# Kernel optimization log

Measured on AMD Instinct MI355X. Metric: run time of the kernel, lower is better.

Reference implementation:

```python
import jax, jax.numpy as jnp
import numpy as np

EPS = 1e-5

def _bn_eval(x, gamma, beta, mean, var):
    return (x - mean) * (gamma / jnp.sqrt(var + EPS)) + beta

def setup_inputs() -> dict:
    key = jax.random.key(0)
    ks = jax.random.split(key, 12)
    N, E, D, C, H = 100000, 1000000, 64, 32, 128
    fused = 4 * D + C  # 288
    z = jax.random.normal(ks[0], (N, D), dtype=jnp.float32)
    edge_index = jax.random.randint(ks[1], (2, E), 0, N, dtype=jnp.int64)
    edge_context = jax.random.normal(ks[2], (E, C), dtype=jnp.float32)
    W1 = jax.random.normal(ks[3], (fused, H), dtype=jnp.float32) / np.sqrt(fused)
    b1 = jnp.zeros((H,), jnp.float32)
    g1 = jnp.ones((H,), jnp.float32); be1 = jnp.zeros((H,), jnp.float32)
    m1 = jnp.zeros((H,), jnp.float32); v1 = jnp.ones((H,), jnp.float32)
    W2 = jax.random.normal(ks[4], (H, H // 2), dtype=jnp.float32) / np.sqrt(H)
    b2 = jnp.zeros((H // 2,), jnp.float32)
    g2 = jnp.ones((H // 2,), jnp.float32); be2 = jnp.zeros((H // 2,), jnp.float32)
    m2 = jnp.zeros((H // 2,), jnp.float32); v2 = jnp.ones((H // 2,), jnp.float32)
    W3 = jax.random.normal(ks[5], (H // 2, 1), dtype=jnp.float32) / np.sqrt(H // 2)
    b3 = jnp.zeros((1,), jnp.float32)
    return {"z": z, "edge_index": edge_index, "edge_context": edge_context,
            "W1": W1, "b1": b1, "g1": g1, "be1": be1, "m1": m1, "v1": v1,
            "W2": W2, "b2": b2, "g2": g2, "be2": be2, "m2": m2, "v2": v2,
            "W3": W3, "b3": b3}

def reference(z, edge_index, edge_context,
              W1, b1, g1, be1, m1, v1,
              W2, b2, g2, be2, m2, v2,
              W3, b3):
    # gather endpoint embeddings: [E, D]
    src = z[edge_index[0]]
    dst = z[edge_index[1]]
    # fused features: [E, 4*D + C]
    fused = jnp.concatenate([src, dst, src * dst, jnp.abs(src - dst), edge_context], axis=1)
    x = jax.nn.relu(_bn_eval(fused @ W1 + b1, g1, be1, m1, v1))
    x = jax.nn.relu(_bn_eval(x @ W2 + b2, g2, be2, m2, v2))
    return (x @ W3 + b3).reshape(-1)
```

## Files before the change

kernel.cpp:

```cpp
#include <hip/hip_runtime.h>
#include <hip/hip_bf16.h>

typedef __attribute__((ext_vector_type(8))) short bf16x8;
typedef __attribute__((ext_vector_type(4))) float f32x4;
typedef __attribute__((ext_vector_type(4))) unsigned int u32x4;
typedef __attribute__((ext_vector_type(2))) unsigned int u32x2;
typedef __attribute__((ext_vector_type(2))) __bf16 bf16x2v;

#define EPS 1e-5f

__device__ inline unsigned short f2bf(float x) {
  unsigned int u = __builtin_bit_cast(unsigned int, x);
  unsigned int r = (u + 0x7FFFu + ((u >> 16) & 1u)) >> 16;
  return (unsigned short)r;
}

__device__ inline unsigned int cvtpk(float a, float b) {
  bf16x2v v = {(__bf16)a, (__bf16)b};
  return __builtin_bit_cast(unsigned int, v);
}

__global__ void prep_kernel(const float* __restrict__ W1, const float* __restrict__ W2,
                            const float* __restrict__ b1, const float* __restrict__ g1,
                            const float* __restrict__ be1, const float* __restrict__ m1,
                            const float* __restrict__ v1,
                            const float* __restrict__ b2, const float* __restrict__ g2,
                            const float* __restrict__ be2, const float* __restrict__ m2,
                            const float* __restrict__ v2,
                            unsigned short* __restrict__ w1f, unsigned short* __restrict__ w2f,
                            float* __restrict__ sc) {
  int t = blockIdx.x * 256 + threadIdx.x;
  if (t < 36864) {
    int j = t & 7, l = (t >> 3) & 63, f = t >> 9;
    int kb = f >> 3, nb = f & 7;
    int rk = kb * 32 + ((l >> 4) << 3) + j;
    int cn = (nb << 4) + (l & 15);
    w1f[t] = f2bf(W1[rk * 128 + cn]);
  } else if (t < 45056) {
    int o = t - 36864;
    int j = o & 7, l = (o >> 3) & 63, f = o >> 9;
    int kb = f >> 2, nb = f & 3;
    int s = kb * 32 + ((l >> 4) << 3) + j;
    int rk = (s & 96) | ((s & 1) << 4) | ((s >> 1) & 15);
    int cn = (nb << 4) + (l & 15);
    w2f[o] = f2bf(W2[rk * 64 + cn]);
  } else if (t < 45184) {
    int j = t - 45056;
    float s = g1[j] * rsqrtf(v1[j] + EPS);
    sc[j] = s;
    sc[128 + j] = (b1[j] - m1[j]) * s + be1[j];
  } else if (t < 45248) {
    int j = t - 45184;
    float s = g2[j] * rsqrtf(v2[j] + EPS);
    sc[256 + j] = s;
    sc[320 + j] = (b2[j] - m2[j]) * s + be2[j];
  }
}

#define LDS_SC_OFF 73728
#define LDS_A_OFF 75776
#define LDS_L3_OFF 157696
#define LDS_TOTAL 158720

#define WRITE_A()                                                                                \
  do {                                                                                           \
    const int rswz_ = (sr & 7) << 4;                                                             \
    char* rowp_ = AR + sr * 640;                                                                 \
    u32x4 ps_ = {cvtpk(sv0[0], sv0[1]), cvtpk(sv0[2], sv0[3]), cvtpk(sv1[0], sv1[1]),            \
                 cvtpk(sv1[2], sv1[3])};                                                         \
    u32x4 pd_ = {cvtpk(dv0[0], dv0[1]), cvtpk(dv0[2], dv0[3]), cvtpk(dv1[0], dv1[1]),            \
                 cvtpk(dv1[2], dv1[3])};                                                         \
    u32x4 pp_ = {cvtpk(sv0[0] * dv0[0], sv0[1] * dv0[1]), cvtpk(sv0[2] * dv0[2], sv0[3] * dv0[3]),\
                 cvtpk(sv1[0] * dv1[0], sv1[1] * dv1[1]), cvtpk(sv1[2] * dv1[2], sv1[3] * dv1[3])};\
    u32x4 pa_ = {cvtpk(fabsf(sv0[0] - dv0[0]), fabsf(sv0[1] - dv0[1])),                          \
                 cvtpk(fabsf(sv0[2] - dv0[2]), fabsf(sv0[3] - dv0[3])),                          \
                 cvtpk(fabsf(sv1[0] - dv1[0]), fabsf(sv1[1] - dv1[1])),                          \
                 cvtpk(fabsf(sv1[2] - dv1[2]), fabsf(sv1[3] - dv1[3]))};                         \
    u32x2 pc_ = {cvtpk(cv[0], cv[1]), cvtpk(cv[2], cv[3])};                                      \
    *(u32x4*)(rowp_ + ((sh * 16) ^ rswz_)) = ps_;                                                \
    *(u32x4*)(rowp_ + ((128 + sh * 16) ^ rswz_)) = pd_;                                          \
    *(u32x4*)(rowp_ + ((256 + sh * 16) ^ rswz_)) = pp_;                                          \
    *(u32x4*)(rowp_ + ((384 + sh * 16) ^ rswz_)) = pa_;                                          \
    *(u32x2*)(rowp_ + 512 + ((sh * 8) ^ rswz_)) = pc_;                                           \
  } while (0)

#define GATHER_NEXT(tg)                                                                          \
  do {                                                                                           \
    const f32x4* zs_ = (const f32x4*)(z + ((size_t)i0n * 64 + sh * 8));                          \
    sv0 = zs_[0];                                                                                \
    sv1 = zs_[1];                                                                                \
    const f32x4* zd_ = (const f32x4*)(z + ((size_t)i1n * 64 + sh * 8));                          \
    dv0 = zd_[0];                                                                                \
    dv1 = zd_[1];                                                                                \
    int eg_ = ((tg) << 7) + sr;                                                                  \
    int esg_ = eg_ < E ? eg_ : E - 1;                                                            \
    cv = *(const f32x4*)(ctx + (size_t)esg_ * 32 + sh * 4);                                      \
    int tn_ = (tg) + grid;                                                                       \
    if (tn_ >= nblk) tn_ = (tg);                                                                 \
    int en_ = (tn_ << 7) + sr;                                                                   \
    int esn_ = en_ < E ? en_ : E - 1;                                                            \
    i0n = ei[esn_];                                                                              \
    i1n = ei[E + esn_];                                                                          \
  } while (0)

__global__ __launch_bounds__(1024, 4) void fused_kernel(
    const float* __restrict__ z, const int* __restrict__ ei, const float* __restrict__ ctx,
    const unsigned short* __restrict__ w1f, const unsigned short* __restrict__ w2f,
    const float* __restrict__ sc, const float* __restrict__ w3, const float* __restrict__ b3,
    float* __restrict__ out, int E, int nblk) {
  extern __shared__ char lds[];
  char* W1L = lds;
  float* SC = (float*)(lds + LDS_SC_OFF);
  char* AR = lds + LDS_A_OFF;
  char* X1 = lds + LDS_A_OFF;
  float* l3 = (float*)(lds + LDS_L3_OFF);

  const int tid = threadIdx.x;
  const int lane = tid & 63, wave = tid >> 6;
  const int g = lane >> 4, lq = lane & 15;
  const int wr = wave >> 2, wc = wave & 3;
  const int w2r = wave >> 1, w2c = wave & 1;
  const int sr = tid >> 3, sh = tid & 7;
  const int grid = gridDim.x;

  {
    const f32x4* s = (const f32x4*)w1f;
    f32x4* d = (f32x4*)W1L;
#pragma unroll
    for (int i = 0; i < 4; i++) d[i * 1024 + tid] = s[i * 1024 + tid];
    if (tid < 512) d[4096 + tid] = s[4096 + tid];
    if (tid < 128) {
      SC[tid] = sc[tid];
      SC[128 + tid] = sc[128 + tid];
    } else if (tid < 192) {
      int j = tid - 128;
      SC[256 + j] = sc[256 + j];
      SC[320 + j] = sc[320 + j];
      SC[384 + j] = w3[j];
    } else if (tid == 192) {
      SC[448] = b3[0];
    }
  }

  bf16x8 w2g0, w2g1, w2g2, w2g3, w2h0, w2h1, w2h2, w2h3;
  {
    const bf16x8* W2G = (const bf16x8*)w2f;
    w2g0 = W2G[(0 * 4 + w2c * 2 + 0) * 64 + lane];
    w2h0 = W2G[(0 * 4 + w2c * 2 + 1) * 64 + lane];
    w2g1 = W2G[(1 * 4 + w2c * 2 + 0) * 64 + lane];
    w2h1 = W2G[(1 * 4 + w2c * 2 + 1) * 64 + lane];
    w2g2 = W2G[(2 * 4 + w2c * 2 + 0) * 64 + lane];
    w2h2 = W2G[(2 * 4 + w2c * 2 + 1) * 64 + lane];
    w2g3 = W2G[(3 * 4 + w2c * 2 + 0) * 64 + lane];
    w2h3 = W2G[(3 * 4 + w2c * 2 + 1) * 64 + lane];
  }

  f32x4 sv0, sv1, dv0, dv1, cv;
  int i0n, i1n;
  int t = blockIdx.x;

  {
    int e = (t << 7) + sr;
    int es = e < E ? e : E - 1;
    int a0 = ei[es], a1 = ei[E + es];
    cv = *(const f32x4*)(ctx + (size_t)es * 32 + sh * 4);
    const f32x4* zs = (const f32x4*)(z + ((size_t)a0 * 64 + sh * 8));
    sv0 = zs[0];
    sv1 = zs[1];
    const f32x4* zd = (const f32x4*)(z + ((size_t)a1 * 64 + sh * 8));
    dv0 = zd[0];
    dv1 = zd[1];
    int tn = t + grid;
    if (tn >= nblk) tn = t;
    int en = (tn << 7) + sr;
    int esn = en < E ? en : E - 1;
    i0n = ei[esn];
    i1n = ei[E + esn];
  }
  WRITE_A();
  {
    int tn = t + grid;
    if (tn >= nblk) tn = t;
    GATHER_NEXT(tn);
  }
  __syncthreads();

  for (; t < nblk; t += grid) {
    f32x4 acc00 = {0.f, 0.f, 0.f, 0.f}, acc01 = acc00, acc10 = acc00, acc11 = acc00;
    const bf16x8* W1F = (const bf16x8*)W1L;
    const int row0 = wr * 32 + lq, row1 = row0 + 16;
    const int swz0 = (row0 & 7) << 4, swz1 = (row1 & 7) << 4;
    const char* ap0 = AR + row0 * 640;
    const char* ap1 = AR + row1 * 640;
#pragma unroll
    for (int kb = 0; kb < 9; kb++) {
      bf16x8 a0 = *(const bf16x8*)(ap0 + ((kb * 64 + g * 16) ^ swz0));
      bf16x8 a1 = *(const bf16x8*)(ap1 + ((kb * 64 + g * 16) ^ swz1));
      bf16x8 b0 = W1F[(kb * 8 + wc * 2 + 0) * 64 + lane];
      bf16x8 b1 = W1F[(kb * 8 + wc * 2 + 1) * 64 + lane];
      acc00 = __builtin_amdgcn_mfma_f32_16x16x32_bf16(a0, b0, acc00, 0, 0, 0);
      acc01 = __builtin_amdgcn_mfma_f32_16x16x32_bf16(a0, b1, acc01, 0, 0, 0);
      acc10 = __builtin_amdgcn_mfma_f32_16x16x32_bf16(a1, b0, acc10, 0, 0, 0);
      acc11 = __builtin_amdgcn_mfma_f32_16x16x32_bf16(a1, b1, acc11, 0, 0, 0);
    }
    __syncthreads();

    {
      const int col0 = wc * 32 + lq, col1 = col0 + 16;
      const float s1v0 = SC[col0], c1v0 = SC[128 + col0];
      const float s1v1 = SC[col1], c1v1 = SC[128 + col1];
      const int xoff = wc * 64 + lq * 4;
#pragma unroll
      for (int j = 0; j < 4; j++) {
        int rowa = wr * 32 + 4 * g + j;
        unsigned int pA = cvtpk(fmaxf(acc00[j] * s1v0 + c1v0, 0.f),
                                fmaxf(acc01[j] * s1v1 + c1v1, 0.f));
        *(unsigned int*)(X1 + rowa * 256 + (xoff ^ ((rowa & 7) << 4))) = pA;
        int rowb = rowa + 16;
        unsigned int pB = cvtpk(fmaxf(acc10[j] * s1v0 + c1v0, 0.f),
                                fmaxf(acc11[j] * s1v1 + c1v1, 0.f));
        *(unsigned int*)(X1 + rowb * 256 + (xoff ^ ((rowb & 7) << 4))) = pB;
      }
    }
    __syncthreads();

    f32x4 acc2A = {0.f, 0.f, 0.f, 0.f}, acc2B = acc2A;
    {
      const int row = w2r * 16 + lq;
      const int swz = (row & 7) << 4;
      const char* xp = X1 + row * 256;
      bf16x8 a0 = *(const bf16x8*)(xp + ((0 * 64 + g * 16) ^ swz));
      acc2A = __builtin_amdgcn_mfma_f32_16x16x32_bf16(a0, w2g0, acc2A, 0, 0, 0);
      acc2B = __builtin_amdgcn_mfma_f32_16x16x32_bf16(a0, w2h0, acc2B, 0, 0, 0);
      bf16x8 a1 = *(const bf16x8*)(xp + ((1 * 64 + g * 16) ^ swz));
      acc2A = __builtin_amdgcn_mfma_f32_16x16x32_bf16(a1, w2g1, acc2A, 0, 0, 0);
      acc2B = __builtin_amdgcn_mfma_f32_16x16x32_bf16(a1, w2h1, acc2B, 0, 0, 0);
      bf16x8 a2 = *(const bf16x8*)(xp + ((2 * 64 + g * 16) ^ swz));
      acc2A = __builtin_amdgcn_mfma_f32_16x16x32_bf16(a2, w2g2, acc2A, 0, 0, 0);
      acc2B = __builtin_amdgcn_mfma_f32_16x16x32_bf16(a2, w2h2, acc2B, 0, 0, 0);
      bf16x8 a3 = *(const bf16x8*)(xp + ((3 * 64 + g * 16) ^ swz));
      acc2A = __builtin_amdgcn_mfma_f32_16x16x32_bf16(a3, w2g3, acc2A, 0, 0, 0);
      acc2B = __builtin_amdgcn_mfma_f32_16x16x32_bf16(a3, w2h3, acc2B, 0, 0, 0);
    }

    const int colA = w2c * 32 + lq, colB = colA + 16;
    const float s2A = SC[256 + colA], c2A = SC[320 + colA];
    const float s2B = SC[256 + colB], c2B = SC[320 + colB];
    const float w3A = SC[384 + colA], w3B = SC[384 + colB];
#pragma unroll
    for (int j = 0; j < 4; j++) {
      float vA = fmaxf(acc2A[j] * s2A + c2A, 0.f);
      float vB = fmaxf(acc2B[j] * s2B + c2B, 0.f);
      float p = vA * w3A + vB * w3B;
      p += __shfl_xor(p, 1);
      p += __shfl_xor(p, 2);
      p += __shfl_xor(p, 4);
      p += __shfl_xor(p, 8);
      if (lq == 0) l3[(w2r * 16 + 4 * g + j) * 2 + w2c] = p;
    }
    __syncthreads();

    WRITE_A();
    {
      int tn2 = t + 2 * grid;
      if (tn2 >= nblk) tn2 = t + grid < nblk ? t + grid : t;
      GATHER_NEXT(tn2);
    }
    if (tid < 128) {
      int e = (t << 7) + tid;
      if (e < E) out[e] = l3[tid * 2] + l3[tid * 2 + 1] + SC[448];
    }
    __syncthreads();
  }
}

extern "C" void kernel_launch(void* const* d_in, const int* in_sizes, int n_in,
                              void* d_out, int out_size, void* d_ws, size_t ws_size,
                              hipStream_t stream) {
  const float* z = (const float*)d_in[0];
  const int* ei = (const int*)d_in[1];
  const float* ctx = (const float*)d_in[2];
  const float* W1 = (const float*)d_in[3];
  const float* b1 = (const float*)d_in[4];
  const float* g1 = (const float*)d_in[5];
  const float* be1 = (const float*)d_in[6];
  const float* m1 = (const float*)d_in[7];
  const float* v1 = (const float*)d_in[8];
  const float* W2 = (const float*)d_in[9];
  const float* b2 = (const float*)d_in[10];
  const float* g2 = (const float*)d_in[11];
  const float* be2 = (const float*)d_in[12];
  const float* m2 = (const float*)d_in[13];
  const float* v2 = (const float*)d_in[14];
  const float* W3 = (const float*)d_in[15];
  const float* b3 = (const float*)d_in[16];
  float* out = (float*)d_out;
  const int E = out_size;

  unsigned short* w1f = (unsigned short*)d_ws;
  unsigned short* w2f = (unsigned short*)((char*)d_ws + 73728);
  float* sc = (float*)((char*)d_ws + 90112);

  prep_kernel<<<177, 256, 0, stream>>>(W1, W2, b1, g1, be1, m1, v1,
                                       b2, g2, be2, m2, v2, w1f, w2f, sc);

  const int nblk = (E + 127) >> 7;
  (void)hipFuncSetAttribute((const void*)fused_kernel,
                            hipFuncAttributeMaxDynamicSharedMemorySize, LDS_TOTAL);
  fused_kernel<<<256, 1024, LDS_TOTAL, stream>>>(z, ei, ctx, w1f, w2f, sc, W3, b3,
                                                 out, E, nblk);
}
```

Baseline: 137.7 us.

## Hold W1 in registers and halve block size with larger per-wave tiles

The W1 fragments move from shared memory into per-wave registers, so the weight matrix is no longer staged in LDS. Blocks shrink from 1024 to 512 threads, and each wave now computes 64 rows by 32 columns for layer 1 and 32 rows for layer 2. Each thread gathers twice as many embedding elements. Layer-1 activation writes are moved after the next-tile gather issue, and one barrier is dropped, so gather latency overlaps with compute. The cost is much higher register pressure (18 W1 plus 8 W2 fragments and 8 accumulators), which could cause spills or lower occupancy.

```diff
diff --git a/kernel.cpp b/kernel.cpp
--- a/kernel.cpp
+++ b/kernel.cpp
@@ -57,44 +57,58 @@
   }
 }
 
-#define LDS_SC_OFF 73728
-#define LDS_A_OFF 75776
-#define LDS_L3_OFF 157696
-#define LDS_TOTAL 158720
+#define LDS_X1_OFF 81920
+#define LDS_SC_OFF 114688
+#define LDS_L3_OFF 116736
+#define LDS_TOTAL 117760
 
 #define WRITE_A()                                                                                \
   do {                                                                                           \
     const int rswz_ = (sr & 7) << 4;                                                             \
     char* rowp_ = AR + sr * 640;                                                                 \
-    u32x4 ps_ = {cvtpk(sv0[0], sv0[1]), cvtpk(sv0[2], sv0[3]), cvtpk(sv1[0], sv1[1]),            \
+    u32x4 s0_ = {cvtpk(sv0[0], sv0[1]), cvtpk(sv0[2], sv0[3]), cvtpk(sv1[0], sv1[1]),            \
                  cvtpk(sv1[2], sv1[3])};                                                         \
-    u32x4 pd_ = {cvtpk(dv0[0], dv0[1]), cvtpk(dv0[2], dv0[3]), cvtpk(dv1[0], dv1[1]),            \
+    u32x4 s1_ = {cvtpk(sv2[0], sv2[1]), cvtpk(sv2[2], sv2[3]), cvtpk(sv3[0], sv3[1]),            \
+                 cvtpk(sv3[2], sv3[3])};                                                         \
+    u32x4 d0_ = {cvtpk(dv0[0], dv0[1]), cvtpk(dv0[2], dv0[3]), cvtpk(dv1[0], dv1[1]),            \
                  cvtpk(dv1[2], dv1[3])};                                                         \
-    u32x4 pp_ = {cvtpk(sv0[0] * dv0[0], sv0[1] * dv0[1]), cvtpk(sv0[2] * dv0[2], sv0[3] * dv0[3]),\
+    u32x4 d1_ = {cvtpk(dv2[0], dv2[1]), cvtpk(dv2[2], dv2[3]), cvtpk(dv3[0], dv3[1]),            \
+                 cvtpk(dv3[2], dv3[3])};                                                         \
+    u32x4 p0_ = {cvtpk(sv0[0] * dv0[0], sv0[1] * dv0[1]), cvtpk(sv0[2] * dv0[2], sv0[3] * dv0[3]),\
                  cvtpk(sv1[0] * dv1[0], sv1[1] * dv1[1]), cvtpk(sv1[2] * dv1[2], sv1[3] * dv1[3])};\
-    u32x4 pa_ = {cvtpk(fabsf(sv0[0] - dv0[0]), fabsf(sv0[1] - dv0[1])),                          \
+    u32x4 p1_ = {cvtpk(sv2[0] * dv2[0], sv2[1] * dv2[1]), cvtpk(sv2[2] * dv2[2], sv2[3] * dv2[3]),\
+                 cvtpk(sv3[0] * dv3[0], sv3[1] * dv3[1]), cvtpk(sv3[2] * dv3[2], sv3[3] * dv3[3])};\
+    u32x4 a0_ = {cvtpk(fabsf(sv0[0] - dv0[0]), fabsf(sv0[1] - dv0[1])),                          \
                  cvtpk(fabsf(sv0[2] - dv0[2]), fabsf(sv0[3] - dv0[3])),                          \
                  cvtpk(fabsf(sv1[0] - dv1[0]), fabsf(sv1[1] - dv1[1])),                          \
                  cvtpk(fabsf(sv1[2] - dv1[2]), fabsf(sv1[3] - dv1[3]))};                         \
-    u32x2 pc_ = {cvtpk(cv[0], cv[1]), cvtpk(cv[2], cv[3])};                                      \
-    *(u32x4*)(rowp_ + ((sh * 16) ^ rswz_)) = ps_;                                                \
-    *(u32x4*)(rowp_ + ((128 + sh * 16) ^ rswz_)) = pd_;                                          \
-    *(u32x4*)(rowp_ + ((256 + sh * 16) ^ rswz_)) = pp_;                                          \
-    *(u32x4*)(rowp_ + ((384 + sh * 16) ^ rswz_)) = pa_;                                          \
-    *(u32x2*)(rowp_ + 512 + ((sh * 8) ^ rswz_)) = pc_;                                           \
+    u32x4 a1_ = {cvtpk(fabsf(sv2[0] - dv2[0]), fabsf(sv2[1] - dv2[1])),                          \
+                 cvtpk(fabsf(sv2[2] - dv2[2]), fabsf(sv2[3] - dv2[3])),                          \
+                 cvtpk(fabsf(sv3[0] - dv3[0]), fabsf(sv3[1] - dv3[1])),                          \
+                 cvtpk(fabsf(sv3[2] - dv3[2]), fabsf(sv3[3] - dv3[3]))};                         \
+    u32x4 c0_ = {cvtpk(cv0[0], cv0[1]), cvtpk(cv0[2], cv0[3]), cvtpk(cv1[0], cv1[1]),            \
+                 cvtpk(cv1[2], cv1[3])};                                                         \
+    *(u32x4*)(rowp_ + ((sh * 32) ^ rswz_)) = s0_;                                                \
+    *(u32x4*)(rowp_ + ((sh * 32 + 16) ^ rswz_)) = s1_;                                           \
+    *(u32x4*)(rowp_ + ((128 + sh * 32) ^ rswz_)) = d0_;                                          \
+    *(u32x4*)(rowp_ + ((128 + sh * 32 + 16) ^ rswz_)) = d1_;                                     \
+    *(u32x4*)(rowp_ + ((256 + sh * 32) ^ rswz_)) = p0_;                                          \
+    *(u32x4*)(rowp_ + ((256 + sh * 32 + 16) ^ rswz_)) = p1_;                                     \
+    *(u32x4*)(rowp_ + ((384 + sh * 32) ^ rswz_)) = a0_;                                          \
+    *(u32x4*)(rowp_ + ((384 + sh * 32 + 16) ^ rswz_)) = a1_;                                     \
+    *(u32x4*)(rowp_ + ((512 + sh * 16) ^ rswz_)) = c0_;                                          \
   } while (0)
 
 #define GATHER_NEXT(tg)                                                                          \
   do {                                                                                           \
-    const f32x4* zs_ = (const f32x4*)(z + ((size_t)i0n * 64 + sh * 8));                          \
-    sv0 = zs_[0];                                                                                \
-    sv1 = zs_[1];                                                                                \
-    const f32x4* zd_ = (const f32x4*)(z + ((size_t)i1n * 64 + sh * 8));                          \
-    dv0 = zd_[0];                                                                                \
-    dv1 = zd_[1];                                                                                \
+    const f32x4* zs_ = (const f32x4*)(z + ((size_t)i0n * 64 + sh * 16));                         \
+    sv0 = zs_[0]; sv1 = zs_[1]; sv2 = zs_[2]; sv3 = zs_[3];                                      \
+    const f32x4* zd_ = (const f32x4*)(z + ((size_t)i1n * 64 + sh * 16));                         \
+    dv0 = zd_[0]; dv1 = zd_[1]; dv2 = zd_[2]; dv3 = zd_[3];                                      \
     int eg_ = ((tg) << 7) + sr;                                                                  \
     int esg_ = eg_ < E ? eg_ : E - 1;                                                            \
-    cv = *(const f32x4*)(ctx + (size_t)esg_ * 32 + sh * 4);                                      \
+    const f32x4* cx_ = (const f32x4*)(ctx + (size_t)esg_ * 32 + sh * 8);                         \
+    cv0 = cx_[0]; cv1 = cx_[1];                                                                  \
     int tn_ = (tg) + grid;                                                                       \
     if (tn_ >= nblk) tn_ = (tg);                                                                 \
     int en_ = (tn_ << 7) + sr;                                                                   \
@@ -103,16 +117,48 @@
     i1n = ei[E + esn_];                                                                          \
   } while (0)
 
-__global__ __launch_bounds__(1024, 4) void fused_kernel(
+#define MFMA16(A, B, C) __builtin_amdgcn_mfma_f32_16x16x32_bf16((A), (B), (C), 0, 0, 0)
+
+#define L1STEP(KB, BB0, BB1)                                                                     \
+  do {                                                                                           \
+    bf16x8 a0_ = *(const bf16x8*)(ap0 + (((KB) * 64 + g * 16) ^ aswz));                          \
+    bf16x8 a1_ = *(const bf16x8*)(ap1 + (((KB) * 64 + g * 16) ^ aswz));                          \
+    bf16x8 a2_ = *(const bf16x8*)(ap2 + (((KB) * 64 + g * 16) ^ aswz));                          \
+    bf16x8 a3_ = *(const bf16x8*)(ap3 + (((KB) * 64 + g * 16) ^ aswz));                          \
+    acc00 = MFMA16(a0_, BB0, acc00); acc01 = MFMA16(a0_, BB1, acc01);                            \
+    acc10 = MFMA16(a1_, BB0, acc10); acc11 = MFMA16(a1_, BB1, acc11);                            \
+    acc20 = MFMA16(a2_, BB0, acc20); acc21 = MFMA16(a2_, BB1, acc21);                            \
+    acc30 = MFMA16(a3_, BB0, acc30); acc31 = MFMA16(a3_, BB1, acc31);                            \
+  } while (0)
+
+#define X1W(MF, ACA, ACB)                                                                        \
+  do {                                                                                           \
+    _Pragma("unroll")                                                                            \
+    for (int j = 0; j < 4; j++) {                                                                \
+      int row_ = wr * 64 + (MF) * 16 + 4 * g + j;                                                \
+      unsigned int p_ = cvtpk(fmaxf(ACA[j] * s1v0 + c1v0, 0.f),                                  \
+                              fmaxf(ACB[j] * s1v1 + c1v1, 0.f));                                 \
+      *(unsigned int*)(X1 + row_ * 256 + (xoff ^ ((row_ & 7) << 4))) = p_;                       \
+    }                                                                                            \
+  } while (0)
+
+#define L2STEP(KB, WG, WH)                                                                       \
+  do {                                                                                           \
+    bf16x8 xa_ = *(const bf16x8*)(xp0 + (((KB) * 64 + g * 16) ^ aswz));                          \
+    bf16x8 xb_ = *(const bf16x8*)(xp1 + (((KB) * 64 + g * 16) ^ aswz));                          \
+    acc2A0 = MFMA16(xa_, WG, acc2A0); acc2A1 = MFMA16(xa_, WH, acc2A1);                          \
+    acc2B0 = MFMA16(xb_, WG, acc2B0); acc2B1 = MFMA16(xb_, WH, acc2B1);                          \
+  } while (0)
+
+__global__ __launch_bounds__(512, 2) void fused_kernel(
     const float* __restrict__ z, const int* __restrict__ ei, const float* __restrict__ ctx,
     const unsigned short* __restrict__ w1f, const unsigned short* __restrict__ w2f,
     const float* __restrict__ sc, const float* __restrict__ w3, const float* __restrict__ b3,
     float* __restrict__ out, int E, int nblk) {
   extern __shared__ char lds[];
-  char* W1L = lds;
+  char* AR = lds;
+  char* X1 = lds + LDS_X1_OFF;
   float* SC = (float*)(lds + LDS_SC_OFF);
-  char* AR = lds + LDS_A_OFF;
-  char* X1 = lds + LDS_A_OFF;
   float* l3 = (float*)(lds + LDS_L3_OFF);
 
   const int tid = threadIdx.x;
@@ -120,42 +166,40 @@
   const int g = lane >> 4, lq = lane & 15;
   const int wr = wave >> 2, wc = wave & 3;
   const int w2r = wave >> 1, w2c = wave & 1;
-  const int sr = tid >> 3, sh = tid & 7;
+  const int sr = tid >> 2, sh = tid & 3;
   const int grid = gridDim.x;
-
-  {
-    const f32x4* s = (const f32x4*)w1f;
-    f32x4* d = (f32x4*)W1L;
-#pragma unroll
-    for (int i = 0; i < 4; i++) d[i * 1024 + tid] = s[i * 1024 + tid];
-    if (tid < 512) d[4096 + tid] = s[4096 + tid];
-    if (tid < 128) {
-      SC[tid] = sc[tid];
-      SC[128 + tid] = sc[128 + tid];
-    } else if (tid < 192) {
-      int j = tid - 128;
-      SC[256 + j] = sc[256 + j];
-      SC[320 + j] = sc[320 + j];
-      SC[384 + j] = w3[j];
-    } else if (tid == 192) {
-      SC[448] = b3[0];
-    }
-  }
-
-  bf16x8 w2g0, w2g1, w2g2, w2g3, w2h0, w2h1, w2h2, w2h3;
-  {
-    const bf16x8* W2G = (const bf16x8*)w2f;
-    w2g0 = W2G[(0 * 4 + w2c * 2 + 0) * 64 + lane];
-    w2h0 = W2G[(0 * 4 + w2c * 2 + 1) * 64 + lane];
-    w2g1 = W2G[(1 * 4 + w2c * 2 + 0) * 64 + lane];
-    w2h1 = W2G[(1 * 4 + w2c * 2 + 1) * 64 + lane];
-    w2g2 = W2G[(2 * 4 + w2c * 2 + 0) * 64 + lane];
-    w2h2 = W2G[(2 * 4 + w2c * 2 + 1) * 64 + lane];
-    w2g3 = W2G[(3 * 4 + w2c * 2 + 0) * 64 + lane];
-    w2h3 = W2G[(3 * 4 + w2c * 2 + 1) * 64 + lane];
-  }
-
-  f32x4 sv0, sv1, dv0, dv1, cv;
+  const int aswz = (lq & 7) << 4;
+
+  if (tid < 128) {
+    SC[tid] = sc[tid];
+    SC[128 + tid] = sc[128 + tid];
+  } else if (tid < 192) {
+    int j = tid - 128;
+    SC[256 + j] = sc[256 + j];
+    SC[320 + j] = sc[320 + j];
+    SC[384 + j] = w3[j];
+  } else if (tid == 192) {
+    SC[448] = b3[0];
+  }
+
+  const bf16x8* W1G = (const bf16x8*)w1f;
+  bf16x8 w1r0 = W1G[(0 * 8 + wc * 2 + 0) * 64 + lane], w1s0 = W1G[(0 * 8 + wc * 2 + 1) * 64 + lane];
+  bf16x8 w1r1 = W1G[(1 * 8 + wc * 2 + 0) * 64 + lane], w1s1 = W1G[(1 * 8 + wc * 2 + 1) * 64 + lane];
+  bf16x8 w1r2 = W1G[(2 * 8 + wc * 2 + 0) * 64 + lane], w1s2 = W1G[(2 * 8 + wc * 2 + 1) * 64 + lane];
+  bf16x8 w1r3 = W1G[(3 * 8 + wc * 2 + 0) * 64 + lane], w1s3 = W1G[(3 * 8 + wc * 2 + 1) * 64 + lane];
+  bf16x8 w1r4 = W1G[(4 * 8 + wc * 2 + 0) * 64 + lane], w1s4 = W1G[(4 * 8 + wc * 2 + 1) * 64 + lane];
+  bf16x8 w1r5 = W1G[(5 * 8 + wc * 2 + 0) * 64 + lane], w1s5 = W1G[(5 * 8 + wc * 2 + 1) * 64 + lane];
+  bf16x8 w1r6 = W1G[(6 * 8 + wc * 2 + 0) * 64 + lane], w1s6 = W1G[(6 * 8 + wc * 2 + 1) * 64 + lane];
+  bf16x8 w1r7 = W1G[(7 * 8 + wc * 2 + 0) * 64 + lane], w1s7 = W1G[(7 * 8 + wc * 2 + 1) * 64 + lane];
+  bf16x8 w1r8 = W1G[(8 * 8 + wc * 2 + 0) * 64 + lane], w1s8 = W1G[(8 * 8 + wc * 2 + 1) * 64 + lane];
+
+  const bf16x8* W2G = (const bf16x8*)w2f;
+  bf16x8 w2g0 = W2G[(0 * 4 + w2c * 2 + 0) * 64 + lane], w2h0 = W2G[(0 * 4 + w2c * 2 + 1) * 64 + lane];
+  bf16x8 w2g1 = W2G[(1 * 4 + w2c * 2 + 0) * 64 + lane], w2h1 = W2G[(1 * 4 + w2c * 2 + 1) * 64 + lane];
+  bf16x8 w2g2 = W2G[(2 * 4 + w2c * 2 + 0) * 64 + lane], w2h2 = W2G[(2 * 4 + w2c * 2 + 1) * 64 + lane];
+  bf16x8 w2g3 = W2G[(3 * 4 + w2c * 2 + 0) * 64 + lane], w2h3 = W2G[(3 * 4 + w2c * 2 + 1) * 64 + lane];
+
+  f32x4 sv0, sv1, sv2, sv3, dv0, dv1, dv2, dv3, cv0, cv1;
   int i0n, i1n;
   int t = blockIdx.x;
 
@@ -163,13 +207,12 @@
     int e = (t << 7) + sr;
     int es = e < E ? e : E - 1;
     int a0 = ei[es], a1 = ei[E + es];
-    cv = *(const f32x4*)(ctx + (size_t)es * 32 + sh * 4);
-    const f32x4* zs = (const f32x4*)(z + ((size_t)a0 * 64 + sh * 8));
-    sv0 = zs[0];
-    sv1 = zs[1];
-    const f32x4* zd = (const f32x4*)(z + ((size_t)a1 * 64 + sh * 8));
-    dv0 = zd[0];
-    dv1 = zd[1];
+    const f32x4* cx = (const f32x4*)(ctx + (size_t)es * 32 + sh * 8);
+    cv0 = cx[0]; cv1 = cx[1];
+    const f32x4* zs = (const f32x4*)(z + ((size_t)a0 * 64 + sh * 16));
+    sv0 = zs[0]; sv1 = zs[1]; sv2 = zs[2]; sv3 = zs[3];
+    const f32x4* zd = (const f32x4*)(z + ((size_t)a1 * 64 + sh * 16));
+    dv0 = zd[0]; dv1 = zd[1]; dv2 = zd[2]; dv3 = zd[3];
     int tn = t + grid;
     if (tn >= nblk) tn = t;
     int en = (tn << 7) + sr;
@@ -187,77 +230,20 @@
 
   for (; t < nblk; t += grid) {
     f32x4 acc00 = {0.f, 0.f, 0.f, 0.f}, acc01 = acc00, acc10 = acc00, acc11 = acc00;
-    const bf16x8* W1F = (const bf16x8*)W1L;
-    const int row0 = wr * 32 + lq, row1 = row0 + 16;
-    const int swz0 = (row0 & 7) << 4, swz1 = (row1 & 7) << 4;
-    const char* ap0 = AR + row0 * 640;
-    const char* ap1 = AR + row1 * 640;
-#pragma unroll
-    for (int kb = 0; kb < 9; kb++) {
-      bf16x8 a0 = *(const bf16x8*)(ap0 + ((kb * 64 + g * 16) ^ swz0));
-      bf16x8 a1 = *(const bf16x8*)(ap1 + ((kb * 64 + g * 16) ^ swz1));
-      bf16x8 b0 = W1F[(kb * 8 + wc * 2 + 0) * 64 + lane];
-      bf16x8 b1 = W1F[(kb * 8 + wc * 2 + 1) * 64 + lane];
-      acc00 = __builtin_amdgcn_mfma_f32_16x16x32_bf16(a0, b0, acc00, 0, 0, 0);
-      acc01 = __builtin_amdgcn_mfma_f32_16x16x32_bf16(a0, b1, acc01, 0, 0, 0);
-      acc10 = __builtin_amdgcn_mfma_f32_16x16x32_bf16(a1, b0, acc10, 0, 0, 0);
-      acc11 = __builtin_amdgcn_mfma_f32_16x16x32_bf16(a1, b1, acc11, 0, 0, 0);
-    }
-    __syncthreads();
-
-    {
-      const int col0 = wc * 32 + lq, col1 = col0 + 16;
-      const float s1v0 = SC[col0], c1v0 = SC[128 + col0];
-      const float s1v1 = SC[col1], c1v1 = SC[128 + col1];
-      const int xoff = wc * 64 + lq * 4;
-#pragma unroll
-      for (int j = 0; j < 4; j++) {
-        int rowa = wr * 32 + 4 * g + j;
-        unsigned int pA = cvtpk(fmaxf(acc00[j] * s1v0 + c1v0, 0.f),
-                                fmaxf(acc01[j] * s1v1 + c1v1, 0.f));
-        *(unsigned int*)(X1 + rowa * 256 + (xoff ^ ((rowa & 7) << 4))) = pA;
-        int rowb = rowa + 16;
-        unsigned int pB = cvtpk(fmaxf(acc10[j] * s1v0 + c1v0, 0.f),
-                                fmaxf(acc11[j] * s1v1 + c1v1, 0.f));
-        *(unsigned int*)(X1 + rowb * 256 + (xoff ^ ((rowb & 7) << 4))) = pB;
-      }
-    }
-    __syncthreads();
-
-    f32x4 acc2A = {0.f, 0.f, 0.f, 0.f}, acc2B = acc2A;
-    {
-      const int row = w2r * 16 + lq;
-      const int swz = (row & 7) << 4;
-      const char* xp = X1 + row * 256;
-      bf16x8 a0 = *(const bf16x8*)(xp + ((0 * 64 + g * 16) ^ swz));
-      acc2A = __builtin_amdgcn_mfma_f32_16x16x32_bf16(a0, w2g0, acc2A, 0, 0, 0);
-      acc2B = __builtin_amdgcn_mfma_f32_16x16x32_bf16(a0, w2h0, acc2B, 0, 0, 0);
-      bf16x8 a1 = *(const bf16x8*)(xp + ((1 * 64 + g * 16) ^ swz));
-      acc2A = __builtin_amdgcn_mfma_f32_16x16x32_bf16(a1, w2g1, acc2A, 0, 0, 0);
-      acc2B = __builtin_amdgcn_mfma_f32_16x16x32_bf16(a1, w2h1, acc2B, 0, 0, 0);
-      bf16x8 a2 = *(const bf16x8*)(xp + ((2 * 64 + g * 16) ^ swz));
-      acc2A = __builtin_amdgcn_mfma_f32_16x16x32_bf16(a2, w2g2, acc2A, 0, 0, 0);
-      acc2B = __builtin_amdgcn_mfma_f32_16x16x32_bf16(a2, w2h2, acc2B, 0, 0, 0);
-      bf16x8 a3 = *(const bf16x8*)(xp + ((3 * 64 + g * 16) ^ swz));
-      acc2A = __builtin_amdgcn_mfma_f32_16x16x32_bf16(a3, w2g3, acc2A, 0, 0, 0);
-      acc2B = __builtin_amdgcn_mfma_f32_16x16x32_bf16(a3, w2h3, acc2B, 0, 0, 0);
-    }
-
-    const int colA = w2c * 32 + lq, colB = colA + 16;
-    const float s2A = SC[256 + colA], c2A = SC[320 + colA];
-    const float s2B = SC[256 + colB], c2B = SC[320 + colB];
-    const float w3A = SC[384 + colA], w3B = SC[384 + colB];
-#pragma unroll
-    for (int j = 0; j < 4; j++) {
-      float vA = fmaxf(acc2A[j] * s2A + c2A, 0.f);
-      float vB = fmaxf(acc2B[j] * s2B + c2B, 0.f);
-      float p = vA * w3A + vB * w3B;
-      p += __shfl_xor(p, 1);
-      p += __shfl_xor(p, 2);
-      p += __shfl_xor(p, 4);
-      p += __shfl_xor(p, 8);
-      if (lq == 0) l3[(w2r * 16 + 4 * g + j) * 2 + w2c] = p;
-    }
+    f32x4 acc20 = acc00, acc21 = acc00, acc30 = acc00, acc31 = acc00;
+    const char* ap0 = AR + (wr * 64 + 0 * 16 + lq) * 640;
+    const char* ap1 = AR + (wr * 64 + 1 * 16 + lq) * 640;
+    const char* ap2 = AR + (wr * 64 + 2 * 16 + lq) * 640;
+    const char* ap3 = AR + (wr * 64 + 3 * 16 + lq) * 640;
+    L1STEP(0, w1r0, w1s0);
+    L1STEP(1, w1r1, w1s1);
+    L1STEP(2, w1r2, w1s2);
+    L1STEP(3, w1r3, w1s3);
+    L1STEP(4, w1r4, w1s4);
+    L1STEP(5, w1r5, w1s5);
+    L1STEP(6, w1r6, w1s6);
+    L1STEP(7, w1r7, w1s7);
+    L1STEP(8, w1r8, w1s8);
     __syncthreads();
 
     WRITE_A();
@@ -266,11 +252,57 @@
       if (tn2 >= nblk) tn2 = t + grid < nblk ? t + grid : t;
       GATHER_NEXT(tn2);
     }
+    {
+      const int col0 = wc * 32 + lq;
+      const float s1v0 = SC[col0], c1v0 = SC[128 + col0];
+      const float s1v1 = SC[col0 + 16], c1v1 = SC[128 + col0 + 16];
+      const int xoff = wc * 64 + lq * 4;
+      X1W(0, acc00, acc01);
+      X1W(1, acc10, acc11);
+      X1W(2, acc20, acc21);
+      X1W(3, acc30, acc31);
+    }
+    __syncthreads();
+
+    f32x4 acc2A0 = {0.f, 0.f, 0.f, 0.f}, acc2A1 = acc2A0, acc2B0 = acc2A0, acc2B1 = acc2A0;
+    const char* xp0 = X1 + (w2r * 32 + lq) * 256;
+    const char* xp1 = xp0 + 4096;
+    L2STEP(0, w2g0, w2h0);
+    L2STEP(1, w2g1, w2h1);
+    L2STEP(2, w2g2, w2h2);
+    L2STEP(3, w2g3, w2h3);
+
+    {
+      const int colA = w2c * 32 + lq, colB = colA + 16;
+      const float s2A = SC[256 + colA], c2A = SC[320 + colA];
+      const float s2B = SC[256 + colB], c2B = SC[320 + colB];
+      const float w3A = SC[384 + colA], w3B = SC[384 + colB];
+#pragma unroll
+      for (int j = 0; j < 4; j++) {
+        float pA = fmaxf(acc2A0[j] * s2A + c2A, 0.f) * w3A +
+                   fmaxf(acc2A1[j] * s2B + c2B, 0.f) * w3B;
+        pA += __shfl_xor(pA, 1);
+        pA += __shfl_xor(pA, 2);
+        pA += __shfl_xor(pA, 4);
+        pA += __shfl_xor(pA, 8);
+        float pB = fmaxf(acc2B0[j] * s2A + c2A, 0.f) * w3A +
+                   fmaxf(acc2B1[j] * s2B + c2B, 0.f) * w3B;
+        pB += __shfl_xor(pB, 1);
+        pB += __shfl_xor(pB, 2);
+        pB += __shfl_xor(pB, 4);
+        pB += __shfl_xor(pB, 8);
+        if (lq == 0) {
+          l3[(w2r * 32 + 4 * g + j) * 2 + w2c] = pA;
+          l3[(w2r * 32 + 16 + 4 * g + j) * 2 + w2c] = pB;
+        }
+      }
+    }
+    __syncthreads();
+
     if (tid < 128) {
       int e = (t << 7) + tid;
       if (e < E) out[e] = l3[tid * 2] + l3[tid * 2 + 1] + SC[448];
     }
-    __syncthreads();
   }
 }
 
@@ -307,6 +339,6 @@
   const int nblk = (E + 127) >> 7;
   (void)hipFuncSetAttribute((const void*)fused_kernel,
                             hipFuncAttributeMaxDynamicSharedMemorySize, LDS_TOTAL);
-  fused_kernel<<<256, 1024, LDS_TOTAL, stream>>>(z, ei, ctx, w1f, w2f, sc, W3, b3,
-                                                 out, E, nblk);
-}
+  fused_kernel<<<256, 512, LDS_TOTAL, stream>>>(z, ei, ctx, w1f, w2f, sc, W3, b3,
+                                                out, E, nblk);
+}
```

Measured after the change: 381.4 us. +176.9%, slower.

## Feed gathered features directly into MFMA registers, skipping LDS staging of layer-1 input

Applied to the files above, without the earlier changes.

Adds a new fused kernel in which each wave gathers endpoint embeddings and edge context straight into the register layout of the MFMA A operand. It builds the src, dst, product and abs-diff features in registers, so the layer-1 input tile is never written to or read back from LDS. The block shrinks to 512 threads with 64 edges per tile, W2 now lives in LDS, and the LDS footprint drops. The launcher picks the new kernel only when it has no register spills and otherwise falls back to the old kernel. The trade-off is more VGPR pressure from the prefetched gather registers and redundant feature building across the four N-group waves.

```diff
diff --git a/kernel.cpp b/kernel.cpp
--- a/kernel.cpp
+++ b/kernel.cpp
@@ -19,6 +19,19 @@
   bf16x2v v = {(__bf16)a, (__bf16)b};
   return __builtin_bit_cast(unsigned int, v);
 }
+
+__device__ inline bf16x8 pk8(f32x4 a, f32x4 b) {
+  u32x4 u = {cvtpk(a[0], a[1]), cvtpk(a[2], a[3]), cvtpk(b[0], b[1]), cvtpk(b[2], b[3])};
+  return __builtin_bit_cast(bf16x8, u);
+}
+
+__device__ inline f32x4 vad(f32x4 a, f32x4 b) {
+  f32x4 r = a - b;
+  r[0] = fabsf(r[0]); r[1] = fabsf(r[1]); r[2] = fabsf(r[2]); r[3] = fabsf(r[3]);
+  return r;
+}
+
+#define MFMA16(A, B, C) __builtin_amdgcn_mfma_f32_16x16x32_bf16((A), (B), (C), 0, 0, 0)
 
 __global__ void prep_kernel(const float* __restrict__ W1, const float* __restrict__ W2,
                             const float* __restrict__ b1, const float* __restrict__ g1,
@@ -57,12 +70,181 @@
   }
 }
 
-#define LDS_SC_OFF 73728
-#define LDS_A_OFF 75776
-#define LDS_L3_OFF 157696
-#define LDS_TOTAL 158720
-
-#define WRITE_A()                                                                                \
+#define R2_X1_OFF 73728
+#define R2_W2_OFF 90112
+#define R2_L3_OFF 106496
+#define R2_LDS_TOTAL 107008
+
+#define GATHER_R2(tg)                                                                            \
+  do {                                                                                           \
+    const f32x4* p0_ = (const f32x4*)(z + (size_t)iN0 * 64 + g * 8);                             \
+    sA0 = p0_[0]; sA1 = p0_[1];                                                                  \
+    const f32x4* p0b_ = (const f32x4*)(z + (size_t)iN0 * 64 + 32 + g * 8);                       \
+    sA2 = p0b_[0]; sA3 = p0b_[1];                                                                \
+    const f32x4* p1_ = (const f32x4*)(z + (size_t)iN1 * 64 + g * 8);                             \
+    dA0 = p1_[0]; dA1 = p1_[1];                                                                  \
+    const f32x4* p1b_ = (const f32x4*)(z + (size_t)iN1 * 64 + 32 + g * 8);                       \
+    dA2 = p1b_[0]; dA3 = p1b_[1];                                                                \
+    const f32x4* p2_ = (const f32x4*)(z + (size_t)iN2 * 64 + g * 8);                             \
+    sB0 = p2_[0]; sB1 = p2_[1];                                                                  \
+    const f32x4* p2b_ = (const f32x4*)(z + (size_t)iN2 * 64 + 32 + g * 8);                       \
+    sB2 = p2b_[0]; sB3 = p2b_[1];                                                                \
+    const f32x4* p3_ = (const f32x4*)(z + (size_t)iN3 * 64 + g * 8);                             \
+    dB0 = p3_[0]; dB1 = p3_[1];                                                                  \
+    const f32x4* p3b_ = (const f32x4*)(z + (size_t)iN3 * 64 + 32 + g * 8);                       \
+    dB2 = p3b_[0]; dB3 = p3b_[1];                                                                \
+    int ea_ = (tg) * 64 + eg * 32 + r;                                                           \
+    int e0c_ = ea_ < E ? ea_ : E - 1;                                                            \
+    int e1c_ = ea_ + 16 < E ? ea_ + 16 : E - 1;                                                  \
+    const f32x4* ca_ = (const f32x4*)(ctx + (size_t)e0c_ * 32 + g * 8);                          \
+    cA = pk8(ca_[0], ca_[1]);                                                                    \
+    const f32x4* cb_ = (const f32x4*)(ctx + (size_t)e1c_ * 32 + g * 8);                          \
+    cB = pk8(cb_[0], cb_[1]);                                                                    \
+    int tn_ = (tg) + grid;                                                                       \
+    if (tn_ >= nblk) tn_ = (tg);                                                                 \
+    int en_ = tn_ * 64 + eg * 32 + r;                                                            \
+    int en0_ = en_ < E ? en_ : E - 1;                                                            \
+    int en1_ = en_ + 16 < E ? en_ + 16 : E - 1;                                                  \
+    iN0 = ei[en0_]; iN1 = ei[E + en0_]; iN2 = ei[en1_]; iN3 = ei[E + en1_];                      \
+  } while (0)
+
+#define L1K_R2(KB, A0X, A1X)                                                                     \
+  do {                                                                                           \
+    bf16x8 b0_ = W1F[((KB) * 8 + ng * 2 + 0) * 64 + lane];                                       \
+    bf16x8 b1_ = W1F[((KB) * 8 + ng * 2 + 1) * 64 + lane];                                       \
+    bf16x8 a0_ = (A0X);                                                                          \
+    bf16x8 a1_ = (A1X);                                                                          \
+    acc00 = MFMA16(a0_, b0_, acc00); acc01 = MFMA16(a0_, b1_, acc01);                            \
+    acc10 = MFMA16(a1_, b0_, acc10); acc11 = MFMA16(a1_, b1_, acc11);                            \
+  } while (0)
+
+__global__ __launch_bounds__(512) void fused_kernel_r2(
+    const float* __restrict__ z, const int* __restrict__ ei, const float* __restrict__ ctx,
+    const unsigned short* __restrict__ w1f, const unsigned short* __restrict__ w2f,
+    const float* __restrict__ sc, const float* __restrict__ w3, const float* __restrict__ b3,
+    float* __restrict__ out, int E, int nblk) {
+  extern __shared__ char lds[];
+  char* W1L = lds;
+  char* X1 = lds + R2_X1_OFF;
+  char* W2L = lds + R2_W2_OFF;
+  float* l3 = (float*)(lds + R2_L3_OFF);
+
+  const int tid = threadIdx.x;
+  const int lane = tid & 63, wave = tid >> 6;
+  const int g = lane >> 4, lq = lane & 15, r = lq;
+  const int eg = wave >> 2, ng = wave & 3;
+  const int w2r = wave >> 1, w2c = wave & 1;
+  const int grid = gridDim.x;
+
+  {
+    const f32x4* s1p = (const f32x4*)w1f;
+    f32x4* d1p = (f32x4*)W1L;
+#pragma unroll
+    for (int i = 0; i < 9; i++) d1p[i * 512 + tid] = s1p[i * 512 + tid];
+    const f32x4* s2p = (const f32x4*)w2f;
+    f32x4* d2p = (f32x4*)W2L;
+    d2p[tid] = s2p[tid];
+    d2p[512 + tid] = s2p[512 + tid];
+  }
+
+  const float s1v0 = sc[ng * 32 + lq], c1v0 = sc[128 + ng * 32 + lq];
+  const float s1v1 = sc[ng * 32 + 16 + lq], c1v1 = sc[128 + ng * 32 + 16 + lq];
+  const int colA = w2c * 32 + lq;
+  const float s2A = sc[256 + colA], c2A = sc[320 + colA];
+  const float s2B = sc[256 + colA + 16], c2B = sc[320 + colA + 16];
+  const float w3A = w3[colA], w3B = w3[colA + 16];
+  const float b3v = b3[0];
+  const int xoff = ng * 64 + lq * 4;
+
+  f32x4 sA0, sA1, sA2, sA3, sB0, sB1, sB2, sB3;
+  f32x4 dA0, dA1, dA2, dA3, dB0, dB1, dB2, dB3;
+  bf16x8 cA, cB;
+  int iN0, iN1, iN2, iN3;
+  int t = blockIdx.x;
+
+  {
+    int ea = t * 64 + eg * 32 + r;
+    int e0c = ea < E ? ea : E - 1;
+    int e1c = ea + 16 < E ? ea + 16 : E - 1;
+    iN0 = ei[e0c]; iN1 = ei[E + e0c]; iN2 = ei[e1c]; iN3 = ei[E + e1c];
+  }
+  GATHER_R2(t);
+  __syncthreads();
+
+  const bf16x8* W1F = (const bf16x8*)W1L;
+  for (; t < nblk; t += grid) {
+    f32x4 acc00 = {0.f, 0.f, 0.f, 0.f}, acc01 = acc00, acc10 = acc00, acc11 = acc00;
+    L1K_R2(0, pk8(sA0, sA1), pk8(sB0, sB1));
+    L1K_R2(1, pk8(sA2, sA3), pk8(sB2, sB3));
+    L1K_R2(2, pk8(dA0, dA1), pk8(dB0, dB1));
+    L1K_R2(3, pk8(dA2, dA3), pk8(dB2, dB3));
+    L1K_R2(4, pk8(sA0 * dA0, sA1 * dA1), pk8(sB0 * dB0, sB1 * dB1));
+    L1K_R2(5, pk8(sA2 * dA2, sA3 * dA3), pk8(sB2 * dB2, sB3 * dB3));
+    L1K_R2(6, pk8(vad(sA0, dA0), vad(sA1, dA1)), pk8(vad(sB0, dB0), vad(sB1, dB1)));
+    L1K_R2(7, pk8(vad(sA2, dA2), vad(sA3, dA3)), pk8(vad(sB2, dB2), vad(sB3, dB3)));
+    L1K_R2(8, cA, cB);
+
+    {
+      int tg = t + grid;
+      if (tg >= nblk) tg = t;
+      GATHER_R2(tg);
+    }
+
+#pragma unroll
+    for (int j = 0; j < 4; j++) {
+      int r0 = eg * 32 + 4 * g + j;
+      unsigned int pA = cvtpk(fmaxf(acc00[j] * s1v0 + c1v0, 0.f),
+                              fmaxf(acc01[j] * s1v1 + c1v1, 0.f));
+      *(unsigned int*)(X1 + r0 * 256 + (xoff ^ ((r0 & 7) << 4))) = pA;
+      int r1 = r0 + 16;
+      unsigned int pB = cvtpk(fmaxf(acc10[j] * s1v0 + c1v0, 0.f),
+                              fmaxf(acc11[j] * s1v1 + c1v1, 0.f));
+      *(unsigned int*)(X1 + r1 * 256 + (xoff ^ ((r1 & 7) << 4))) = pB;
+    }
+    __syncthreads();
+
+    f32x4 acc2A = {0.f, 0.f, 0.f, 0.f}, acc2B = acc2A;
+    {
+      const int row = w2r * 16 + lq;
+      const int swz = (row & 7) << 4;
+      const char* xp = X1 + row * 256;
+      const bf16x8* W2F = (const bf16x8*)W2L;
+#pragma unroll
+      for (int kb = 0; kb < 4; kb++) {
+        bf16x8 a2 = *(const bf16x8*)(xp + ((kb * 64 + g * 16) ^ swz));
+        bf16x8 bg = W2F[(kb * 4 + w2c * 2 + 0) * 64 + lane];
+        bf16x8 bh = W2F[(kb * 4 + w2c * 2 + 1) * 64 + lane];
+        acc2A = MFMA16(a2, bg, acc2A);
+        acc2B = MFMA16(a2, bh, acc2B);
+      }
+    }
+
+#pragma unroll
+    for (int j = 0; j < 4; j++) {
+      float vA = fmaxf(acc2A[j] * s2A + c2A, 0.f);
+      float vB = fmaxf(acc2B[j] * s2B + c2B, 0.f);
+      float p = vA * w3A + vB * w3B;
+      p += __shfl_xor(p, 1);
+      p += __shfl_xor(p, 2);
+      p += __shfl_xor(p, 4);
+      p += __shfl_xor(p, 8);
+      if (lq == 0) l3[(w2r * 16 + 4 * g + j) * 2 + w2c] = p;
+    }
+    __syncthreads();
+
+    if (tid < 64) {
+      int e = t * 64 + tid;
+      if (e < E) out[e] = l3[tid * 2] + l3[tid * 2 + 1] + b3v;
+    }
+  }
+}
+
+#define F_SC_OFF 73728
+#define F_A_OFF 75776
+#define F_L3_OFF 157696
+#define F_LDS_TOTAL 158720
+
+#define WRITE_A_F()                                                                              \
   do {                                                                                           \
     const int rswz_ = (sr & 7) << 4;                                                             \
     char* rowp_ = AR + sr * 640;                                                                 \
@@ -84,7 +266,7 @@
     *(u32x2*)(rowp_ + 512 + ((sh * 8) ^ rswz_)) = pc_;                                           \
   } while (0)
 
-#define GATHER_NEXT(tg)                                                                          \
+#define GATHER_NEXT_F(tg)                                                                        \
   do {                                                                                           \
     const f32x4* zs_ = (const f32x4*)(z + ((size_t)i0n * 64 + sh * 8));                          \
     sv0 = zs_[0];                                                                                \
@@ -103,17 +285,17 @@
     i1n = ei[E + esn_];                                                                          \
   } while (0)
 
-__global__ __launch_bounds__(1024, 4) void fused_kernel(
+__global__ __launch_bounds__(1024, 4) void fused_kernel_f(
     const float* __restrict__ z, const int* __restrict__ ei, const float* __restrict__ ctx,
     const unsigned short* __restrict__ w1f, const unsigned short* __restrict__ w2f,
     const float* __restrict__ sc, const float* __restrict__ w3, const float* __restrict__ b3,
     float* __restrict__ out, int E, int nblk) {
   extern __shared__ char lds[];
   char* W1L = lds;
-  float* SC = (float*)(lds + LDS_SC_OFF);
-  char* AR = lds + LDS_A_OFF;
-  char* X1 = lds + LDS_A_OFF;
-  float* l3 = (float*)(lds + LDS_L3_OFF);
+  float* SC = (float*)(lds + F_SC_OFF);
+  char* AR = lds + F_A_OFF;
+  char* X1 = lds + F_A_OFF;
+  float* l3 = (float*)(lds + F_L3_OFF);
 
   const int tid = threadIdx.x;
   const int lane = tid & 63, wave = tid >> 6;
@@ -177,11 +359,11 @@
     i0n = ei[esn];
     i1n = ei[E + esn];
   }
-  WRITE_A();
+  WRITE_A_F();
   {
     int tn = t + grid;
     if (tn >= nblk) tn = t;
-    GATHER_NEXT(tn);
+    GATHER_NEXT_F(tn);
   }
   __syncthreads();
 
@@ -198,17 +380,17 @@
       bf16x8 a1 = *(const bf16x8*)(ap1 + ((kb * 64 + g * 16) ^ swz1));
       bf16x8 b0 = W1F[(kb * 8 + wc * 2 + 0) * 64 + lane];
       bf16x8 b1 = W1F[(kb * 8 + wc * 2 + 1) * 64 + lane];
-      acc00 = __builtin_amdgcn_mfma_f32_16x16x32_bf16(a0, b0, acc00, 0, 0, 0);
-      acc01 = __builtin_amdgcn_mfma_f32_16x16x32_bf16(a0, b1, acc01, 0, 0, 0);
-      acc10 = __builtin_amdgcn_mfma_f32_16x16x32_bf16(a1, b0, acc10, 0, 0, 0);
-      acc11 = __builtin_amdgcn_mfma_f32_16x16x32_bf16(a1, b1, acc11, 0, 0, 0);
+      acc00 = MFMA16(a0, b0, acc00);
+      acc01 = MFMA16(a0, b1, acc01);
+      acc10 = MFMA16(a1, b0, acc10);
+      acc11 = MFMA16(a1, b1, acc11);
     }
     __syncthreads();
 
     {
-      const int col0 = wc * 32 + lq, col1 = col0 + 16;
+      const int col0 = wc * 32 + lq;
       const float s1v0 = SC[col0], c1v0 = SC[128 + col0];
-      const float s1v1 = SC[col1], c1v1 = SC[128 + col1];
+      const float s1v1 = SC[col0 + 16], c1v1 = SC[128 + col0 + 16];
       const int xoff = wc * 64 + lq * 4;
 #pragma unroll
       for (int j = 0; j < 4; j++) {
@@ -230,17 +412,17 @@
       const int swz = (row & 7) << 4;
       const char* xp = X1 + row * 256;
       bf16x8 a0 = *(const bf16x8*)(xp + ((0 * 64 + g * 16) ^ swz));
-      acc2A = __builtin_amdgcn_mfma_f32_16x16x32_bf16(a0, w2g0, acc2A, 0, 0, 0);
-      acc2B = __builtin_amdgcn_mfma_f32_16x16x32_bf16(a0, w2h0, acc2B, 0, 0, 0);
+      acc2A = MFMA16(a0, w2g0, acc2A);
+      acc2B = MFMA16(a0, w2h0, acc2B);
       bf16x8 a1 = *(const bf16x8*)(xp + ((1 * 64 + g * 16) ^ swz));
-      acc2A = __builtin_amdgcn_mfma_f32_16x16x32_bf16(a1, w2g1, acc2A, 0, 0, 0);
-      acc2B = __builtin_amdgcn_mfma_f32_16x16x32_bf16(a1, w2h1, acc2B, 0, 0, 0);
+      acc2A = MFMA16(a1, w2g1, acc2A);
+      acc2B = MFMA16(a1, w2h1, acc2B);
       bf16x8 a2 = *(const bf16x8*)(xp + ((2 * 64 + g * 16) ^ swz));
-      acc2A = __builtin_amdgcn_mfma_f32_16x16x32_bf16(a2, w2g2, acc2A, 0, 0, 0);
-      acc2B = __builtin_amdgcn_mfma_f32_16x16x32_bf16(a2, w2h2, acc2B, 0, 0, 0);
+      acc2A = MFMA16(a2, w2g2, acc2A);
+      acc2B = MFMA16(a2, w2h2, acc2B);
       bf16x8 a3 = *(const bf16x8*)(xp + ((3 * 64 + g * 16) ^ swz));
-      acc2A = __builtin_amdgcn_mfma_f32_16x16x32_bf16(a3, w2g3, acc2A, 0, 0, 0);
-      acc2B = __builtin_amdgcn_mfma_f32_16x16x32_bf16(a3, w2h3, acc2B, 0, 0, 0);
+      acc2A = MFMA16(a3, w2g3, acc2A);
+      acc2B = MFMA16(a3, w2h3, acc2B);
     }
 
     const int colA = w2c * 32 + lq, colB = colA + 16;
@@ -260,11 +442,11 @@
     }
     __syncthreads();
 
-    WRITE_A();
+    WRITE_A_F();
     {
       int tn2 = t + 2 * grid;
       if (tn2 >= nblk) tn2 = t + grid < nblk ? t + grid : t;
-      GATHER_NEXT(tn2);
+      GATHER_NEXT_F(tn2);
     }
     if (tid < 128) {
       int e = (t << 7) + tid;
@@ -304,9 +486,23 @@
   prep_kernel<<<177, 256, 0, stream>>>(W1, W2, b1, g1, be1, m1, v1,
                                        b2, g2, be2, m2, v2, w1f, w2f, sc);
 
-  const int nblk = (E + 127) >> 7;
-  (void)hipFuncSetAttribute((const void*)fused_kernel,
-                            hipFuncAttributeMaxDynamicSharedMemorySize, LDS_TOTAL);
-  fused_kernel<<<256, 1024, LDS_TOTAL, stream>>>(z, ei, ctx, w1f, w2f, sc, W3, b3,
-                                                 out, E, nblk);
-}
+  hipFuncAttributes attr;
+  bool use_r2 = false;
+  if (hipFuncGetAttributes(&attr, (const void*)fused_kernel_r2) == hipSuccess) {
+    use_r2 = (attr.localSizeBytes < 16);
+  }
+
+  if (use_r2) {
+    const int nblk = (E + 63) >> 6;
+    (void)hipFuncSetAttribute((const void*)fused_kernel_r2,
+                              hipFuncAttributeMaxDynamicSharedMemorySize, R2_LDS_TOTAL);
+    fused_kernel_r2<<<256, 512, R2_LDS_TOTAL, stream>>>(z, ei, ctx, w1f, w2f, sc, W3, b3,
+                                                        out, E, nblk);
+  } else {
+    const int nblk = (E + 127) >> 7;
+    (void)hipFuncSetAttribute((const void*)fused_kernel_f,
+                              hipFuncAttributeMaxDynamicSharedMemorySize, F_LDS_TOTAL);
+    fused_kernel_f<<<256, 1024, F_LDS_TOTAL, stream>>>(z, ei, ctx, w1f, w2f, sc, W3, b3,
+                                                       out, E, nblk);
+  }
+}
```

Result: slower. 320.7 us (+132.8%).
